# Kernel optimization log

Hardware: AMD Instinct MI355X
Metric: run time of the kernel (lower is better)

Reference implementation:

```python
import jax, jax.numpy as jnp
import numpy as np

D, N, M = 256, 8192, 8192
DISTANCE_THRESH = 0.8


def setup_inputs() -> dict:
    key = jax.random.key(0)
    k0, k1 = jax.random.split(key)
    d0 = jax.random.normal(k0, (D, N), dtype=jnp.float32)
    d1 = jax.random.normal(k1, (D, M), dtype=jnp.float32)
    # descriptors are L2-normalized along the feature dim (cosine similarity,
    # consistent with the 2*(1-sim) squared-distance formula in the module)
    d0 = d0 / jnp.linalg.norm(d0, axis=0, keepdims=True)
    d1 = d1 / jnp.linalg.norm(d1, axis=0, keepdims=True)
    return {"descriptors0": d0, "descriptors1": d1}


def reference(descriptors0, descriptors1):
    # nn_sim: [N, M] similarity matrix
    nn_sim = jnp.einsum('dn,dm->nm', descriptors0, descriptors1)
    nn_dist_01 = jnp.max(nn_sim, axis=1)          # [N]
    nn_idx_01 = jnp.argmax(nn_sim, axis=1)        # [N]
    nn_idx_10 = jnp.argmax(nn_sim, axis=0)        # [M]
    nn_dist = 2.0 * (1.0 - nn_dist_01)            # squared L2 dist for unit vecs
    ids1 = jnp.arange(nn_sim.shape[0])
    mask = ids1 == nn_idx_10[nn_idx_01]           # mutual NN check
    if DISTANCE_THRESH > 0.0:
        mask = mask & (nn_dist <= DISTANCE_THRESH ** 2)
    matches = jnp.where(mask, nn_idx_01, -1)
    scores = jnp.where(mask, (nn_dist + 1.0) / 2.0, 0.0)
    return matches, scores
```

## Files before the change

### kernel.cpp

```cpp
#include <hip/hip_runtime.h>
#include <hip/hip_bf16.h>

typedef __attribute__((ext_vector_type(8))) short short8;
typedef __attribute__((ext_vector_type(4))) float floatx4;
typedef unsigned int u32;

#define D_DIM 256
#define TCOLS 32
#define TILES 16
#define IDX_BITS 0x1FFFu
#define VAL_MASK 0xFFFFE000u


__device__ inline unsigned short f2bf_rne(float f) {
  u32 u = __float_as_uint(f);
  u32 r = (u + 0x7FFFu + ((u >> 16) & 1u)) >> 16;
  return (unsigned short)r;
}

__device__ inline u32 umax(u32 a, u32 b) { return a > b ? a : b; }

__device__ inline void async_ld16(const void* g, void* l) {
  __builtin_amdgcn_global_load_lds((const __attribute__((address_space(1))) void*)g,
                                   (__attribute__((address_space(3))) void*)l, 16, 0, 0);
}


__global__ __launch_bounds__(256) void transpose_cast(const float* __restrict__ src,
                                                      unsigned short* __restrict__ dst, int C,
                                                      u32* __restrict__ best, int init_n) {
  const int tid = threadIdx.x;
  const int d = blockIdx.x * 64 + (tid & 63);
  const int chunk = blockIdx.y * 4 + (tid >> 6);
  const int f0 = chunk * 8;
  float v[8];
#pragma unroll
  for (int u = 0; u < 8; ++u) v[u] = src[(size_t)(f0 + u) * C + d];
  short8 o;
#pragma unroll
  for (int u = 0; u < 8; ++u) o[u] = (short)f2bf_rne(v[u]);
  *(short8*)(dst + (size_t)d * D_DIM + f0) = o;
  if (blockIdx.y == 0) {
    int i = blockIdx.x * 256 + tid;
    if (i < init_n) best[i] = 0u;
  }
}

__global__ __launch_bounds__(256, 1) void gemm_reduce(const float* __restrict__ A,
                                                      const unsigned short* __restrict__ Bt,
                                                      u32* __restrict__ best01,
                                                      u32* __restrict__ best10,
                                                      int N) {
  __shared__ alignas(16) unsigned short sB[2][TCOLS * D_DIM];

  const int tid  = threadIdx.x;
  const int wave = tid >> 6;
  const int lane = tid & 63;
  const int quad = lane >> 4;
  const int l15  = lane & 15;
  const int n0   = blockIdx.x * 256;
  const int mg0  = blockIdx.y * (TILES * TCOLS);
  const int rbase = n0 + wave * 64;

  {
    const unsigned short* src = Bt + (size_t)mg0 * D_DIM;
#pragma unroll
    for (int c = 0; c < 4; ++c) {
      int slot = c * 256 + tid;
      int r = slot >> 5, cc = slot & 31;
      int ccg = (cc & 24) | ((cc ^ r) & 7);
      async_ld16(src + (size_t)r * D_DIM + ccg * 8, (unsigned short*)sB[0] + slot * 8);
    }
  }

  short8 af[4][8];
#pragma unroll
  for (int t = 0; t < 4; ++t)
#pragma unroll
    for (int kc = 0; kc < 8; ++kc) {
      const int row = rbase + t * 16 + l15;
      const int kb = kc * 32 + quad * 8;
      short8 o;
#pragma unroll
      for (int u = 0; u < 8; ++u)
        o[u] = (short)f2bf_rne(A[(size_t)(kb + u) * N + row]);
      af[t][kc] = o;
    }

  u32 rbk[16];
#pragma unroll
  for (int s = 0; s < 16; ++s) rbk[s] = 0u;

  __syncthreads();

  for (int mt = 0; mt < TILES; ++mt) {
    const int m0 = mg0 + mt * TCOLS;
    if (mt + 1 < TILES) {
      const unsigned short* src = Bt + (size_t)(m0 + TCOLS) * D_DIM;
      unsigned short* dstb = (unsigned short*)sB[(mt + 1) & 1];
#pragma unroll
      for (int c = 0; c < 4; ++c) {
        int slot = c * 256 + tid;
        int r = slot >> 5, cc = slot & 31;
        int ccg = (cc & 24) | ((cc ^ r) & 7);
        async_ld16(src + (size_t)r * D_DIM + ccg * 8, dstb + slot * 8);
      }
    }

    floatx4 acc[4][2];
#pragma unroll
    for (int i = 0; i < 4; ++i)
#pragma unroll
      for (int j = 0; j < 2; ++j)
        acc[i][j] = (floatx4){2.0f, 2.0f, 2.0f, 2.0f};

    const unsigned short* sb = (const unsigned short*)sB[mt & 1];
#pragma unroll
    for (int kc = 0; kc < 8; ++kc) {
      short8 bfr[2];
#pragma unroll
      for (int j = 0; j < 2; ++j) {
        int c2 = j * 16 + l15;
        int ch = kc * 4 + quad;
        int chg = (ch & 24) | ((ch ^ c2) & 7);
        bfr[j] = *(const short8*)(sb + c2 * D_DIM + chg * 8);
      }
#pragma unroll
      for (int i = 0; i < 4; ++i)
#pragma unroll
        for (int j = 0; j < 2; ++j)
          acc[i][j] = __builtin_amdgcn_mfma_f32_16x16x32_bf16(af[i][kc], bfr[j], acc[i][j], 0, 0, 0);
    }

    u32 cb[2] = {0u, 0u};
    u32 colpay[2];
#pragma unroll
    for (int j = 0; j < 2; ++j) colpay[j] = (~(u32)(m0 + j * 16 + l15)) & IDX_BITS;
#pragma unroll
    for (int i = 0; i < 4; ++i)
#pragma unroll
      for (int r = 0; r < 4; ++r) {
        u32 rowpay = (~(u32)(rbase + i * 16 + quad * 4 + r)) & IDX_BITS;
        u32 rb = rbk[i * 4 + r];
#pragma unroll
        for (int j = 0; j < 2; ++j) {
          u32 u = __float_as_uint(acc[i][j][r]) & VAL_MASK;
          rb = umax(rb, u | colpay[j]);
          cb[j] = umax(cb[j], u | rowpay);
        }
        rbk[i * 4 + r] = rb;
      }
#pragma unroll
    for (int j = 0; j < 2; ++j) {
      u32 b = cb[j];
      b = umax(b, (u32)__shfl_xor((int)b, 16, 64));
      b = umax(b, (u32)__shfl_xor((int)b, 32, 64));
      if (quad == 0) atomicMax(&best10[m0 + j * 16 + l15], b);
    }
    __syncthreads();
  }

#pragma unroll
  for (int i = 0; i < 4; ++i)
#pragma unroll
    for (int r = 0; r < 4; ++r) {
      u32 b = rbk[i * 4 + r];
      b = umax(b, (u32)__shfl_xor((int)b, 1, 64));
      b = umax(b, (u32)__shfl_xor((int)b, 2, 64));
      b = umax(b, (u32)__shfl_xor((int)b, 4, 64));
      b = umax(b, (u32)__shfl_xor((int)b, 8, 64));
      if (l15 == 0) atomicMax(&best01[rbase + i * 16 + quad * 4 + r], b);
    }
}

__global__ void finalize(const u32* __restrict__ best01, const u32* __restrict__ best10,
                         float* __restrict__ out, int N) {
  int n = blockIdx.x * blockDim.x + threadIdx.x;
  if (n >= N) return;
  u32 k = best01[n];
  int idx01 = (int)((~k) & IDX_BITS);
  float sim = __uint_as_float(k & VAL_MASK) - 2.0f;
  int idx10 = (int)((~best10[idx01]) & IDX_BITS);
  float dist = 2.0f - 2.0f * sim;
  bool ok = (idx10 == n) && (dist <= 0.64f);
  out[n]     = ok ? (float)idx01 : -1.0f;
  out[N + n] = ok ? 1.5f - sim : 0.0f;
}


extern "C" void kernel_launch(void* const* d_in, const int* in_sizes, int n_in,
                              void* d_out, int out_size, void* d_ws, size_t ws_size,
                              hipStream_t stream) {
  (void)n_in; (void)out_size; (void)ws_size;
  const float* d0 = (const float*)d_in[0];
  const float* d1 = (const float*)d_in[1];
  const int N = in_sizes[0] / D_DIM;
  const int M = in_sizes[1] / D_DIM;

  u32* best01 = (u32*)d_ws;
  u32* best10 = best01 + N;
  unsigned short* Bt = (unsigned short*)(best10 + M);
  float* out = (float*)d_out;

  hipLaunchKernelGGL(transpose_cast, dim3(M / 64, 8), dim3(256), 0, stream,
                     d1, Bt, M, best01, N + M);
  hipLaunchKernelGGL(gemm_reduce, dim3(N / 256, M / (TILES * TCOLS)), dim3(256), 0, stream,
                     d0, Bt, best01, best10, N);
  hipLaunchKernelGGL(finalize, dim3(N / 256), dim3(256), 0, stream, best01, best10, out, N);
}
```

Measured before the change: 103.7 us.

## Load B fragments directly from global memory instead of LDS double buffering

Removes the LDS staging of B tiles, the async global-to-LDS prefetch, the swizzle and the per-tile block barrier. Each wave now reads its B fragments straight from global memory into registers. This drops synchronization and LDS traffic, but every wave fetches B redundantly and loses the prefetch overlap, relying on L1/L2 caching to hide latency.

```diff
diff --git a/kernel.cpp b/kernel.cpp
--- a/kernel.cpp
+++ b/kernel.cpp
@@ -18,12 +18,7 @@
   return (unsigned short)r;
 }
 
-__device__ inline u32 umax(u32 a, u32 b) { return a > b ? a : b; }
-
-__device__ inline void async_ld16(const void* g, void* l) {
-  __builtin_amdgcn_global_load_lds((const __attribute__((address_space(1))) void*)g,
-                                   (__attribute__((address_space(3))) void*)l, 16, 0, 0);
-}
+__device__ inline u32 umax_(u32 a, u32 b) { return a > b ? a : b; }
 
 
 __global__ __launch_bounds__(256) void transpose_cast(const float* __restrict__ src,
@@ -31,8 +26,7 @@
                                                       u32* __restrict__ best, int init_n) {
   const int tid = threadIdx.x;
   const int d = blockIdx.x * 64 + (tid & 63);
-  const int chunk = blockIdx.y * 4 + (tid >> 6);
-  const int f0 = chunk * 8;
+  const int f0 = (blockIdx.y * 4 + (tid >> 6)) * 8;
   float v[8];
 #pragma unroll
   for (int u = 0; u < 8; ++u) v[u] = src[(size_t)(f0 + u) * C + d];
@@ -51,8 +45,6 @@
                                                       u32* __restrict__ best01,
                                                       u32* __restrict__ best10,
                                                       int N) {
-  __shared__ alignas(16) unsigned short sB[2][TCOLS * D_DIM];
-
   const int tid  = threadIdx.x;
   const int wave = tid >> 6;
   const int lane = tid & 63;
@@ -61,17 +53,6 @@
   const int n0   = blockIdx.x * 256;
   const int mg0  = blockIdx.y * (TILES * TCOLS);
   const int rbase = n0 + wave * 64;
-
-  {
-    const unsigned short* src = Bt + (size_t)mg0 * D_DIM;
-#pragma unroll
-    for (int c = 0; c < 4; ++c) {
-      int slot = c * 256 + tid;
-      int r = slot >> 5, cc = slot & 31;
-      int ccg = (cc & 24) | ((cc ^ r) & 7);
-      async_ld16(src + (size_t)r * D_DIM + ccg * 8, (unsigned short*)sB[0] + slot * 8);
-    }
-  }
 
   short8 af[4][8];
 #pragma unroll
@@ -91,21 +72,10 @@
 #pragma unroll
   for (int s = 0; s < 16; ++s) rbk[s] = 0u;
 
-  __syncthreads();
+  const unsigned short* blane = Bt + (size_t)(mg0 + l15) * D_DIM + quad * 8;
 
   for (int mt = 0; mt < TILES; ++mt) {
     const int m0 = mg0 + mt * TCOLS;
-    if (mt + 1 < TILES) {
-      const unsigned short* src = Bt + (size_t)(m0 + TCOLS) * D_DIM;
-      unsigned short* dstb = (unsigned short*)sB[(mt + 1) & 1];
-#pragma unroll
-      for (int c = 0; c < 4; ++c) {
-        int slot = c * 256 + tid;
-        int r = slot >> 5, cc = slot & 31;
-        int ccg = (cc & 24) | ((cc ^ r) & 7);
-        async_ld16(src + (size_t)r * D_DIM + ccg * 8, dstb + slot * 8);
-      }
-    }
 
     floatx4 acc[4][2];
 #pragma unroll
@@ -114,17 +84,13 @@
       for (int j = 0; j < 2; ++j)
         acc[i][j] = (floatx4){2.0f, 2.0f, 2.0f, 2.0f};
 
-    const unsigned short* sb = (const unsigned short*)sB[mt & 1];
+    const unsigned short* bt0 = blane + (size_t)mt * TCOLS * D_DIM;
 #pragma unroll
     for (int kc = 0; kc < 8; ++kc) {
       short8 bfr[2];
 #pragma unroll
-      for (int j = 0; j < 2; ++j) {
-        int c2 = j * 16 + l15;
-        int ch = kc * 4 + quad;
-        int chg = (ch & 24) | ((ch ^ c2) & 7);
-        bfr[j] = *(const short8*)(sb + c2 * D_DIM + chg * 8);
-      }
+      for (int j = 0; j < 2; ++j)
+        bfr[j] = *(const short8*)(bt0 + (size_t)j * 16 * D_DIM + kc * 32);
 #pragma unroll
       for (int i = 0; i < 4; ++i)
 #pragma unroll
@@ -145,19 +111,18 @@
 #pragma unroll
         for (int j = 0; j < 2; ++j) {
           u32 u = __float_as_uint(acc[i][j][r]) & VAL_MASK;
-          rb = umax(rb, u | colpay[j]);
-          cb[j] = umax(cb[j], u | rowpay);
+          rb = umax_(rb, u | colpay[j]);
+          cb[j] = umax_(cb[j], u | rowpay);
         }
         rbk[i * 4 + r] = rb;
       }
 #pragma unroll
     for (int j = 0; j < 2; ++j) {
       u32 b = cb[j];
-      b = umax(b, (u32)__shfl_xor((int)b, 16, 64));
-      b = umax(b, (u32)__shfl_xor((int)b, 32, 64));
+      b = umax_(b, (u32)__shfl_xor((int)b, 16, 64));
+      b = umax_(b, (u32)__shfl_xor((int)b, 32, 64));
       if (quad == 0) atomicMax(&best10[m0 + j * 16 + l15], b);
     }
-    __syncthreads();
   }
 
 #pragma unroll
@@ -165,10 +130,10 @@
 #pragma unroll
     for (int r = 0; r < 4; ++r) {
       u32 b = rbk[i * 4 + r];
-      b = umax(b, (u32)__shfl_xor((int)b, 1, 64));
-      b = umax(b, (u32)__shfl_xor((int)b, 2, 64));
-      b = umax(b, (u32)__shfl_xor((int)b, 4, 64));
-      b = umax(b, (u32)__shfl_xor((int)b, 8, 64));
+      b = umax_(b, (u32)__shfl_xor((int)b, 1, 64));
+      b = umax_(b, (u32)__shfl_xor((int)b, 2, 64));
+      b = umax_(b, (u32)__shfl_xor((int)b, 4, 64));
+      b = umax_(b, (u32)__shfl_xor((int)b, 8, 64));
       if (l15 == 0) atomicMax(&best01[rbase + i * 16 + quad * 4 + r], b);
     }
 }
```

After: 138.2 us. +33.3%, slower.
